# Kernel tuning notes

Measured on AMD Instinct MI355X. Metric: run time of the kernel, lower is better.

The kernel has to match this reference:

```python
import jax, jax.numpy as jnp
import numpy as np

B = 256        # graphs in batch
N_PER = 512    # nodes per graph (uniform)
D = 256        # in_dim
DEG = 16       # avg degree
RATIO = 0.5


def setup_inputs() -> dict:
    key = jax.random.key(0)
    k1, k2, k3, k4 = jax.random.split(key, 4)
    N = B * N_PER
    e_per = N_PER * DEG
    x = jax.random.normal(k1, (N, D), dtype=jnp.float32)
    # edges confined within each graph (DGL batched-graph structure)
    src = jax.random.randint(k2, (B, e_per), 0, N_PER)
    dst = jax.random.randint(k3, (B, e_per), 0, N_PER)
    offs = jnp.arange(B, dtype=jnp.int32)[:, None] * N_PER
    src = (src + offs).reshape(-1).astype(jnp.int32)
    dst = (dst + offs).reshape(-1).astype(jnp.int32)
    W = jax.random.normal(k4, (D, 1), dtype=jnp.float32) / np.sqrt(D)
    b = jnp.zeros((1,), dtype=jnp.float32)
    num_nodes = jnp.full((B,), N_PER, dtype=jnp.int32)
    return {"x": x, "W": W, "b": b, "src": src, "dst": dst, "num_nodes": num_nodes}


def reference(x, W, b, src, dst, num_nodes):
    N, d = x.shape
    bsz = num_nodes.shape[0]
    n = N // bsz                     # uniform nodes per graph -> static
    k = int(np.ceil(RATIO * n))      # nodes kept per graph (static)

    # ---- GraphConv(in_dim, 1), DGL default norm='both':
    # score = D_in^{-1/2} A D_out^{-1/2} (x W) + b   (W applied first: out_dim < in_dim)
    ones_e = jnp.ones(src.shape, dtype=x.dtype)
    deg_out = jax.ops.segment_sum(ones_e, src, num_segments=N)
    deg_in = jax.ops.segment_sum(ones_e, dst, num_segments=N)
    h = x @ W                                              # [N, 1]
    h = h * jax.lax.rsqrt(jnp.clip(deg_out, 1.0))[:, None]
    agg = jax.ops.segment_sum(h[src], dst, num_segments=N) # [N, 1]
    score = (agg * jax.lax.rsqrt(jnp.clip(deg_in, 1.0))[:, None] + b)[:, 0]  # [N]

    # ---- topk per graph: dense [B, n] buffer is just a reshape (uniform graphs),
    # sort descending + take first k  ==  lax.top_k
    dense = score.reshape(bsz, n)
    _, idx = jax.lax.top_k(dense, k)                       # [B, k] descending
    perm = (idx + jnp.arange(bsz)[:, None] * n).reshape(-1)  # global node ids [B*k]

    # ---- gather + scale: feature[perm] * tanh(score[perm])
    feat = x[perm] * jnp.tanh(score[perm])[:, None]        # [B*k, D]

    # ---- node_subgraph: edges whose both endpoints survive
    keep = jnp.zeros((N,), dtype=bool).at[perm].set(True)
    edge_mask = keep[src] & keep[dst]                      # [E]
    next_num_nodes = jnp.full((bsz,), k, dtype=jnp.int32)
    return feat, perm, edge_mask, next_num_nodes
```

## Files before the change

kernel.cpp:

```cpp
#include <hip/hip_runtime.h>
#include <math.h>

#define BB    256
#define NPER  512
#define DD    256
#define KK    256
#define EPG   (NPER * 16)
#define NN    (BB * NPER)
#define EE    (BB * EPG)

__global__ __launch_bounds__(256) void k_dot(const float* __restrict__ x,
                                             const float* __restrict__ W,
                                             float* __restrict__ hraw) {
    const int wave = threadIdx.x >> 6;
    const int lane = threadIdx.x & 63;
    const int r0   = blockIdx.x * 16 + wave * 4;
    const float4 wv = ((const float4*)W)[lane];
    const float4* p = (const float4*)(x + ((size_t)r0 << 8));
    float4 a0 = p[lane];
    float4 a1 = p[64 + lane];
    float4 a2 = p[128 + lane];
    float4 a3 = p[192 + lane];
    float d0 = a0.x * wv.x + a0.y * wv.y + a0.z * wv.z + a0.w * wv.w;
    float d1 = a1.x * wv.x + a1.y * wv.y + a1.z * wv.z + a1.w * wv.w;
    float d2 = a2.x * wv.x + a2.y * wv.y + a2.z * wv.z + a2.w * wv.w;
    float d3 = a3.x * wv.x + a3.y * wv.y + a3.z * wv.z + a3.w * wv.w;
    #pragma unroll
    for (int off = 32; off > 0; off >>= 1) {
        d0 += __shfl_down(d0, off, 64);
        d1 += __shfl_down(d1, off, 64);
        d2 += __shfl_down(d2, off, 64);
        d3 += __shfl_down(d3, off, 64);
    }
    if (lane == 0) {
        hraw[r0]     = d0;
        hraw[r0 + 1] = d1;
        hraw[r0 + 2] = d2;
        hraw[r0 + 3] = d3;
    }
}

__global__ __launch_bounds__(1024) void k_graph(
        const float* __restrict__ x,
        const float* __restrict__ hraw, const float* __restrict__ b,
        const int* __restrict__ src, const int* __restrict__ dst,
        float* __restrict__ feat, float* __restrict__ out_perm,
        float* __restrict__ emask, float* __restrict__ nnn) {
    __shared__ unsigned int es2[EPG / 2];
    __shared__ unsigned int ed2[EPG / 2];
    __shared__ int   degs[NPER];
    __shared__ int   degd[NPER];
    __shared__ float hl[NPER];
    __shared__ float aggl[NPER];
    __shared__ float scl[NPER];
    __shared__ unsigned long long keys[NPER];
    __shared__ float keepf[NPER];
    __shared__ int   sel[KK];
    __shared__ float tsv[KK];

    const int g = blockIdx.x;
    const int t = threadIdx.x;
    const int wave = t >> 6;
    const int lane = t & 63;
    const int nbase = g << 9;

    float hv = (t < NPER) ? hraw[nbase + t] : 0.0f;

    if (t < NPER) { degs[t] = 0; degd[t] = 0; aggl[t] = 0.0f; keepf[t] = 0.0f; }
    __syncthreads();

    const int4* s4 = (const int4*)(src + (size_t)g * EPG);
    const int4* d4 = (const int4*)(dst + (size_t)g * EPG);
    int4 sva = s4[t], dva = d4[t];
    int4 svb = s4[t + 1024], dvb = d4[t + 1024];
    {
        unsigned int a0 = (unsigned int)(sva.x - nbase), a1 = (unsigned int)(sva.y - nbase);
        unsigned int a2 = (unsigned int)(sva.z - nbase), a3 = (unsigned int)(sva.w - nbase);
        es2[t * 2]     = a0 | (a1 << 16);
        es2[t * 2 + 1] = a2 | (a3 << 16);
        atomicAdd(&degs[a0], 1); atomicAdd(&degs[a1], 1);
        atomicAdd(&degs[a2], 1); atomicAdd(&degs[a3], 1);
        unsigned int c0 = (unsigned int)(dva.x - nbase), c1 = (unsigned int)(dva.y - nbase);
        unsigned int c2 = (unsigned int)(dva.z - nbase), c3 = (unsigned int)(dva.w - nbase);
        ed2[t * 2]     = c0 | (c1 << 16);
        ed2[t * 2 + 1] = c2 | (c3 << 16);
        atomicAdd(&degd[c0], 1); atomicAdd(&degd[c1], 1);
        atomicAdd(&degd[c2], 1); atomicAdd(&degd[c3], 1);
    }
    {
        int i = t + 1024;
        unsigned int a0 = (unsigned int)(svb.x - nbase), a1 = (unsigned int)(svb.y - nbase);
        unsigned int a2 = (unsigned int)(svb.z - nbase), a3 = (unsigned int)(svb.w - nbase);
        es2[i * 2]     = a0 | (a1 << 16);
        es2[i * 2 + 1] = a2 | (a3 << 16);
        atomicAdd(&degs[a0], 1); atomicAdd(&degs[a1], 1);
        atomicAdd(&degs[a2], 1); atomicAdd(&degs[a3], 1);
        unsigned int c0 = (unsigned int)(dvb.x - nbase), c1 = (unsigned int)(dvb.y - nbase);
        unsigned int c2 = (unsigned int)(dvb.z - nbase), c3 = (unsigned int)(dvb.w - nbase);
        ed2[i * 2]     = c0 | (c1 << 16);
        ed2[i * 2 + 1] = c2 | (c3 << 16);
        atomicAdd(&degd[c0], 1); atomicAdd(&degd[c1], 1);
        atomicAdd(&degd[c2], 1); atomicAdd(&degd[c3], 1);
    }
    __syncthreads();

    if (t < NPER) hl[t] = hv * rsqrtf(fmaxf((float)degs[t], 1.0f));
    __syncthreads();

    #pragma unroll
    for (int i = t; i < EPG / 2; i += 1024) {
        unsigned int sp = es2[i], dp = ed2[i];
        atomicAdd(&aggl[dp & 0xFFFFu], hl[sp & 0xFFFFu]);
        atomicAdd(&aggl[dp >> 16],     hl[sp >> 16]);
    }
    __syncthreads();

    unsigned long long key = 0;
    if (t < NPER) {
        float sc = aggl[t] * rsqrtf(fmaxf((float)degd[t], 1.0f)) + b[0];
        scl[t] = sc;
        unsigned int u = __float_as_uint(sc);
        u = (u & 0x80000000u) ? ~u : (u | 0x80000000u);
        key = ((unsigned long long)u << 32) |
              (unsigned long long)(0xFFFFFFFFu - (unsigned)t);
    }
    __syncthreads();

    for (int kk = 2; kk <= NPER; kk <<= 1) {
        for (int j = kk >> 1; j > 0; j >>= 1) {
            if (j >= 64) {
                __syncthreads();
                if (t < NPER) keys[t] = key;
                __syncthreads();
                if (t < NPER) {
                    unsigned long long c = keys[t ^ j];
                    bool lower = ((t & j) == 0);
                    bool up    = ((t & kk) == 0);
                    bool takeMax = (up == lower);
                    key = takeMax ? (key >= c ? key : c)
                                  : (key >= c ? c : key);
                }
            } else {
                if (t < NPER) {
                    unsigned long long c = __shfl_xor(key, j, 64);
                    bool lower = ((t & j) == 0);
                    bool up    = ((t & kk) == 0);
                    bool takeMax = (up == lower);
                    key = takeMax ? (key >= c ? key : c)
                                  : (key >= c ? c : key);
                }
            }
        }
    }

    if (t < KK) {
        int idx = (int)(0xFFFFFFFFu - (unsigned int)(key & 0xFFFFFFFFull));
        out_perm[(g << 8) + t] = (float)(nbase + idx);
        sel[t] = idx;
        tsv[t] = tanhf(scl[idx]);
        keepf[idx] = 1.0f;
    }
    __syncthreads();

    #pragma unroll
    for (int it = 0; it < 16; it += 2) {
        const int j0 = wave * 16 + it, j1 = j0 + 1;
        const int l0 = sel[j0], l1 = sel[j1];
        const float s0 = tsv[j0], s1 = tsv[j1];
        const float4* q0 = (const float4*)(x + ((size_t)(nbase + l0) << 8));
        const float4* q1 = (const float4*)(x + ((size_t)(nbase + l1) << 8));
        float4 v0 = q0[lane], v1 = q1[lane];
        float4 o0 = make_float4(v0.x * s0, v0.y * s0, v0.z * s0, v0.w * s0);
        float4 o1 = make_float4(v1.x * s1, v1.y * s1, v1.z * s1, v1.w * s1);
        ((float4*)(feat + ((size_t)((g << 8) + j0) << 8)))[lane] = o0;
        ((float4*)(feat + ((size_t)((g << 8) + j1) << 8)))[lane] = o1;
    }

    float4* em4 = (float4*)(emask + ((size_t)g << 13));
    #pragma unroll
    for (int i = t; i < EPG / 4; i += 1024) {
        unsigned int sp0 = es2[i * 2], sp1 = es2[i * 2 + 1];
        unsigned int dp0 = ed2[i * 2], dp1 = ed2[i * 2 + 1];
        float4 m;
        m.x = keepf[sp0 & 0xFFFFu] * keepf[dp0 & 0xFFFFu];
        m.y = keepf[sp0 >> 16]     * keepf[dp0 >> 16];
        m.z = keepf[sp1 & 0xFFFFu] * keepf[dp1 & 0xFFFFu];
        m.w = keepf[sp1 >> 16]     * keepf[dp1 >> 16];
        em4[i] = m;
    }
    if (g == 0 && t < BB) nnn[t] = (float)KK;
}

extern "C" void kernel_launch(void* const* d_in, const int* in_sizes, int n_in,
                              void* d_out, int out_size, void* d_ws, size_t ws_size,
                              hipStream_t stream) {
    const float* x   = (const float*)d_in[0];
    const float* W   = (const float*)d_in[1];
    const float* b   = (const float*)d_in[2];
    const int*   src = (const int*)d_in[3];
    const int*   dst = (const int*)d_in[4];

    float* out   = (float*)d_out;
    float* feat  = out;
    float* operm = feat + (size_t)BB * KK * DD;
    float* emask = operm + (size_t)BB * KK;
    float* nnn   = emask + (size_t)EE;

    float* hraw = (float*)d_ws;

    k_dot  <<<NN / 16, 256, 0, stream>>>(x, W, hraw);
    k_graph<<<BB, 1024, 0, stream>>>(x, hraw, b, src, dst,
                                     feat, operm, emask, nnn);
}
```

Before: 254.1 us.

## Fuse projection dot into per-graph kernel and use nontemporal output stores

Drops the separate x@W kernel. Each per-graph block now computes its 512 node projections directly into shared memory before building degrees, which removes a launch and the hraw workspace round trip. The feature and edge-mask outputs are written with nontemporal stores to reduce cache pollution. The risk is fewer, heavier blocks: 256 blocks each stream 512 KB of x, which may lower memory parallelism compared with the wide standalone dot kernel. The later gather may also miss more in L2.

```diff
diff --git a/kernel.cpp b/kernel.cpp
--- a/kernel.cpp
+++ b/kernel.cpp
@@ -9,40 +9,12 @@
 #define NN    (BB * NPER)
 #define EE    (BB * EPG)
 
-__global__ __launch_bounds__(256) void k_dot(const float* __restrict__ x,
-                                             const float* __restrict__ W,
-                                             float* __restrict__ hraw) {
-    const int wave = threadIdx.x >> 6;
-    const int lane = threadIdx.x & 63;
-    const int r0   = blockIdx.x * 16 + wave * 4;
-    const float4 wv = ((const float4*)W)[lane];
-    const float4* p = (const float4*)(x + ((size_t)r0 << 8));
-    float4 a0 = p[lane];
-    float4 a1 = p[64 + lane];
-    float4 a2 = p[128 + lane];
-    float4 a3 = p[192 + lane];
-    float d0 = a0.x * wv.x + a0.y * wv.y + a0.z * wv.z + a0.w * wv.w;
-    float d1 = a1.x * wv.x + a1.y * wv.y + a1.z * wv.z + a1.w * wv.w;
-    float d2 = a2.x * wv.x + a2.y * wv.y + a2.z * wv.z + a2.w * wv.w;
-    float d3 = a3.x * wv.x + a3.y * wv.y + a3.z * wv.z + a3.w * wv.w;
-    #pragma unroll
-    for (int off = 32; off > 0; off >>= 1) {
-        d0 += __shfl_down(d0, off, 64);
-        d1 += __shfl_down(d1, off, 64);
-        d2 += __shfl_down(d2, off, 64);
-        d3 += __shfl_down(d3, off, 64);
-    }
-    if (lane == 0) {
-        hraw[r0]     = d0;
-        hraw[r0 + 1] = d1;
-        hraw[r0 + 2] = d2;
-        hraw[r0 + 3] = d3;
-    }
-}
-
-__global__ __launch_bounds__(1024) void k_graph(
+typedef float vf4 __attribute__((ext_vector_type(4)));
+
+__global__ __launch_bounds__(1024) void k_fused(
         const float* __restrict__ x,
-        const float* __restrict__ hraw, const float* __restrict__ b,
+        const float* __restrict__ W,
+        const float* __restrict__ b,
         const int* __restrict__ src, const int* __restrict__ dst,
         float* __restrict__ feat, float* __restrict__ out_perm,
         float* __restrict__ emask, float* __restrict__ nnn) {
@@ -64,15 +36,45 @@
     const int lane = t & 63;
     const int nbase = g << 9;
 
-    float hv = (t < NPER) ? hraw[nbase + t] : 0.0f;
-
-    if (t < NPER) { degs[t] = 0; degd[t] = 0; aggl[t] = 0.0f; keepf[t] = 0.0f; }
-    __syncthreads();
-
     const int4* s4 = (const int4*)(src + (size_t)g * EPG);
     const int4* d4 = (const int4*)(dst + (size_t)g * EPG);
     int4 sva = s4[t], dva = d4[t];
     int4 svb = s4[t + 1024], dvb = d4[t + 1024];
+
+    if (t < NPER) { degs[t] = 0; degd[t] = 0; aggl[t] = 0.0f; keepf[t] = 0.0f; }
+
+    {
+        const float4 wv = ((const float4*)W)[lane];
+        const float4* xb = (const float4*)(x + ((size_t)(nbase + (wave << 5)) << 8));
+        #pragma unroll
+        for (int it = 0; it < 8; ++it) {
+            const float4* p = xb + (it << 8);
+            float4 a0 = p[lane];
+            float4 a1 = p[64 + lane];
+            float4 a2 = p[128 + lane];
+            float4 a3 = p[192 + lane];
+            float d0 = a0.x * wv.x + a0.y * wv.y + a0.z * wv.z + a0.w * wv.w;
+            float d1 = a1.x * wv.x + a1.y * wv.y + a1.z * wv.z + a1.w * wv.w;
+            float d2 = a2.x * wv.x + a2.y * wv.y + a2.z * wv.z + a2.w * wv.w;
+            float d3 = a3.x * wv.x + a3.y * wv.y + a3.z * wv.z + a3.w * wv.w;
+            #pragma unroll
+            for (int off = 32; off > 0; off >>= 1) {
+                d0 += __shfl_down(d0, off, 64);
+                d1 += __shfl_down(d1, off, 64);
+                d2 += __shfl_down(d2, off, 64);
+                d3 += __shfl_down(d3, off, 64);
+            }
+            if (lane == 0) {
+                const int r = (wave << 5) + (it << 2);
+                hl[r]     = d0;
+                hl[r + 1] = d1;
+                hl[r + 2] = d2;
+                hl[r + 3] = d3;
+            }
+        }
+    }
+    __syncthreads();
+
     {
         unsigned int a0 = (unsigned int)(sva.x - nbase), a1 = (unsigned int)(sva.y - nbase);
         unsigned int a2 = (unsigned int)(sva.z - nbase), a3 = (unsigned int)(sva.w - nbase);
@@ -104,7 +106,7 @@
     }
     __syncthreads();
 
-    if (t < NPER) hl[t] = hv * rsqrtf(fmaxf((float)degs[t], 1.0f));
+    if (t < NPER) hl[t] = hl[t] * rsqrtf(fmaxf((float)degs[t], 1.0f));
     __syncthreads();
 
     #pragma unroll
@@ -170,23 +172,25 @@
         const float4* q0 = (const float4*)(x + ((size_t)(nbase + l0) << 8));
         const float4* q1 = (const float4*)(x + ((size_t)(nbase + l1) << 8));
         float4 v0 = q0[lane], v1 = q1[lane];
-        float4 o0 = make_float4(v0.x * s0, v0.y * s0, v0.z * s0, v0.w * s0);
-        float4 o1 = make_float4(v1.x * s1, v1.y * s1, v1.z * s1, v1.w * s1);
-        ((float4*)(feat + ((size_t)((g << 8) + j0) << 8)))[lane] = o0;
-        ((float4*)(feat + ((size_t)((g << 8) + j1) << 8)))[lane] = o1;
-    }
-
-    float4* em4 = (float4*)(emask + ((size_t)g << 13));
+        vf4 o0 = { v0.x * s0, v0.y * s0, v0.z * s0, v0.w * s0 };
+        vf4 o1 = { v1.x * s1, v1.y * s1, v1.z * s1, v1.w * s1 };
+        vf4* f0 = (vf4*)(feat + ((size_t)((g << 8) + j0) << 8)) + lane;
+        vf4* f1 = (vf4*)(feat + ((size_t)((g << 8) + j1) << 8)) + lane;
+        __builtin_nontemporal_store(o0, f0);
+        __builtin_nontemporal_store(o1, f1);
+    }
+
+    vf4* em4 = (vf4*)(emask + ((size_t)g << 13));
     #pragma unroll
     for (int i = t; i < EPG / 4; i += 1024) {
         unsigned int sp0 = es2[i * 2], sp1 = es2[i * 2 + 1];
         unsigned int dp0 = ed2[i * 2], dp1 = ed2[i * 2 + 1];
-        float4 m;
+        vf4 m;
         m.x = keepf[sp0 & 0xFFFFu] * keepf[dp0 & 0xFFFFu];
         m.y = keepf[sp0 >> 16]     * keepf[dp0 >> 16];
         m.z = keepf[sp1 & 0xFFFFu] * keepf[dp1 & 0xFFFFu];
         m.w = keepf[sp1 >> 16]     * keepf[dp1 >> 16];
-        em4[i] = m;
+        __builtin_nontemporal_store(m, &em4[i]);
     }
     if (g == 0 && t < BB) nnn[t] = (float)KK;
 }
@@ -206,9 +210,6 @@
     float* emask = operm + (size_t)BB * KK;
     float* nnn   = emask + (size_t)EE;
 
-    float* hraw = (float*)d_ws;
-
-    k_dot  <<<NN / 16, 256, 0, stream>>>(x, W, hraw);
-    k_graph<<<BB, 1024, 0, stream>>>(x, hraw, b, src, dst,
+    k_fused<<<BB, 1024, 0, stream>>>(x, W, b, src, dst,
                                      feat, operm, emask, nnn);
 }
```

After: 254.6 us. Within noise of the previous version (+0.2%).

## Split feature gather into separate wide-grid kernel with nontemporal stores

Applied to the files above, without the earlier changes.

Moves the x[perm]*tanh(score) gather out of the per-graph 1024-thread kernel into a new kernel with 8192 small blocks. Perm and tanh values pass through global workspace. The per-graph kernel launches only 256 blocks, so the aim is to spread the large gather/write traffic across the whole GPU. Edge-mask and feature writes now use nontemporal stores, and the src/dst loads are issued before the LDS init barrier. The cost is an extra launch, an extra round trip for perm and tanh through global memory, and a float-to-int conversion of perm indices.

```diff
diff --git a/kernel.cpp b/kernel.cpp
--- a/kernel.cpp
+++ b/kernel.cpp
@@ -8,6 +8,8 @@
 #define EPG   (NPER * 16)
 #define NN    (BB * NPER)
 #define EE    (BB * EPG)
+
+typedef float vf4 __attribute__((ext_vector_type(4)));
 
 __global__ __launch_bounds__(256) void k_dot(const float* __restrict__ x,
                                              const float* __restrict__ W,
@@ -41,10 +43,9 @@
 }
 
 __global__ __launch_bounds__(1024) void k_graph(
-        const float* __restrict__ x,
         const float* __restrict__ hraw, const float* __restrict__ b,
         const int* __restrict__ src, const int* __restrict__ dst,
-        float* __restrict__ feat, float* __restrict__ out_perm,
+        float* __restrict__ out_perm, float* __restrict__ tsvg,
         float* __restrict__ emask, float* __restrict__ nnn) {
     __shared__ unsigned int es2[EPG / 2];
     __shared__ unsigned int ed2[EPG / 2];
@@ -55,24 +56,20 @@
     __shared__ float scl[NPER];
     __shared__ unsigned long long keys[NPER];
     __shared__ float keepf[NPER];
-    __shared__ int   sel[KK];
-    __shared__ float tsv[KK];
 
     const int g = blockIdx.x;
     const int t = threadIdx.x;
-    const int wave = t >> 6;
-    const int lane = t & 63;
     const int nbase = g << 9;
-
-    float hv = (t < NPER) ? hraw[nbase + t] : 0.0f;
-
-    if (t < NPER) { degs[t] = 0; degd[t] = 0; aggl[t] = 0.0f; keepf[t] = 0.0f; }
-    __syncthreads();
 
     const int4* s4 = (const int4*)(src + (size_t)g * EPG);
     const int4* d4 = (const int4*)(dst + (size_t)g * EPG);
     int4 sva = s4[t], dva = d4[t];
     int4 svb = s4[t + 1024], dvb = d4[t + 1024];
+    float hv = (t < NPER) ? hraw[nbase + t] : 0.0f;
+
+    if (t < NPER) { degs[t] = 0; degd[t] = 0; aggl[t] = 0.0f; keepf[t] = 0.0f; }
+    __syncthreads();
+
     {
         unsigned int a0 = (unsigned int)(sva.x - nbase), a1 = (unsigned int)(sva.y - nbase);
         unsigned int a2 = (unsigned int)(sva.z - nbase), a3 = (unsigned int)(sva.w - nbase);
@@ -156,39 +153,54 @@
     if (t < KK) {
         int idx = (int)(0xFFFFFFFFu - (unsigned int)(key & 0xFFFFFFFFull));
         out_perm[(g << 8) + t] = (float)(nbase + idx);
-        sel[t] = idx;
-        tsv[t] = tanhf(scl[idx]);
+        tsvg[(g << 8) + t] = tanhf(scl[idx]);
         keepf[idx] = 1.0f;
     }
     __syncthreads();
 
-    #pragma unroll
-    for (int it = 0; it < 16; it += 2) {
-        const int j0 = wave * 16 + it, j1 = j0 + 1;
-        const int l0 = sel[j0], l1 = sel[j1];
-        const float s0 = tsv[j0], s1 = tsv[j1];
-        const float4* q0 = (const float4*)(x + ((size_t)(nbase + l0) << 8));
-        const float4* q1 = (const float4*)(x + ((size_t)(nbase + l1) << 8));
-        float4 v0 = q0[lane], v1 = q1[lane];
-        float4 o0 = make_float4(v0.x * s0, v0.y * s0, v0.z * s0, v0.w * s0);
-        float4 o1 = make_float4(v1.x * s1, v1.y * s1, v1.z * s1, v1.w * s1);
-        ((float4*)(feat + ((size_t)((g << 8) + j0) << 8)))[lane] = o0;
-        ((float4*)(feat + ((size_t)((g << 8) + j1) << 8)))[lane] = o1;
-    }
-
-    float4* em4 = (float4*)(emask + ((size_t)g << 13));
+    vf4* em4 = (vf4*)(emask + ((size_t)g << 13));
     #pragma unroll
     for (int i = t; i < EPG / 4; i += 1024) {
         unsigned int sp0 = es2[i * 2], sp1 = es2[i * 2 + 1];
         unsigned int dp0 = ed2[i * 2], dp1 = ed2[i * 2 + 1];
-        float4 m;
+        vf4 m;
         m.x = keepf[sp0 & 0xFFFFu] * keepf[dp0 & 0xFFFFu];
         m.y = keepf[sp0 >> 16]     * keepf[dp0 >> 16];
         m.z = keepf[sp1 & 0xFFFFu] * keepf[dp1 & 0xFFFFu];
         m.w = keepf[sp1 >> 16]     * keepf[dp1 >> 16];
-        em4[i] = m;
+        __builtin_nontemporal_store(m, &em4[i]);
     }
     if (g == 0 && t < BB) nnn[t] = (float)KK;
+}
+
+__global__ __launch_bounds__(256) void k_feat(
+        const float* __restrict__ x,
+        const float* __restrict__ operm, const float* __restrict__ tsvg,
+        float* __restrict__ feat) {
+    __shared__ int   rsel[8];
+    __shared__ float rts[8];
+    const int blk = blockIdx.x;
+    const int g   = blk >> 5;
+    const int r0  = (blk & 31) << 3;
+    const int t = threadIdx.x;
+    const int wave = t >> 6;
+    const int lane = t & 63;
+    if (t < 8) {
+        const int gr = (g << 8) + r0 + t;
+        rsel[t] = (int)operm[gr];
+        rts[t]  = tsvg[gr];
+    }
+    __syncthreads();
+    #pragma unroll
+    for (int u = 0; u < 2; ++u) {
+        const int j = (wave << 1) + u;
+        const int row = rsel[j];
+        const float s = rts[j];
+        float4 v = ((const float4*)(x + ((size_t)row << 8)))[lane];
+        vf4 o = { v.x * s, v.y * s, v.z * s, v.w * s };
+        __builtin_nontemporal_store(
+            o, (vf4*)(feat + ((size_t)((g << 8) + r0 + j) << 8)) + lane);
+    }
 }
 
 extern "C" void kernel_launch(void* const* d_in, const int* in_sizes, int n_in,
@@ -207,8 +219,10 @@
     float* nnn   = emask + (size_t)EE;
 
     float* hraw = (float*)d_ws;
+    float* tsvg = hraw + NN;
 
     k_dot  <<<NN / 16, 256, 0, stream>>>(x, W, hraw);
-    k_graph<<<BB, 1024, 0, stream>>>(x, hraw, b, src, dst,
-                                     feat, operm, emask, nnn);
-}
+    k_graph<<<BB, 1024, 0, stream>>>(hraw, b, src, dst,
+                                     operm, tsvg, emask, nnn);
+    k_feat <<<(BB * KK) / 8, 256, 0, stream>>>(x, operm, tsvg, feat);
+}
```

Result: no change. 256.0 us (+0.7%).
